# Kernel tuning notes

Measured on AMD Instinct MI355X. Metric: run time of the kernel, lower is better.

The kernel has to match this reference:

```python
import jax, jax.numpy as jnp
import numpy as np

N = 16384   # number of nodes == output_dim
E = 524288  # directed edges (avg degree 32)
IN_DIM, HID = 16, 128


def _glorot(key, shape):
    fan_in = shape[0]
    return jax.random.normal(key, shape, dtype=jnp.float32) / jnp.sqrt(jnp.float32(fan_in))


def setup_inputs() -> dict:
    key = jax.random.key(0)
    ks = jax.random.split(key, 6)
    x = jax.random.normal(ks[0], (N, IN_DIM), dtype=jnp.float32)
    edge_index = jax.random.randint(ks[1], (2, E), 0, N, dtype=jnp.int64)
    return {
        "x": x,
        "edge_index": edge_index,
        "W1": _glorot(ks[2], (IN_DIM, HID)), "b1": jnp.zeros((HID,), jnp.float32),
        "W2": _glorot(ks[3], (HID, HID)),    "b2": jnp.zeros((HID,), jnp.float32),
        "W3": _glorot(ks[4], (HID, HID)),    "b3": jnp.zeros((HID,), jnp.float32),
        "Wfc": _glorot(ks[5], (HID, N)),     "bfc": jnp.zeros((N,), jnp.float32),
    }


def _gcn_conv(x, W, b, src, dst, norm):
    # GCNConv: h = D^{-1/2} (A + I) D^{-1/2} (x @ W) + b
    h = x @ W                              # [N, out]
    msg = h[src] * norm[:, None]           # gather + per-edge scale
    agg = jax.ops.segment_sum(msg, dst, num_segments=N)  # scatter-add to targets
    return agg + b


def reference(x, edge_index, W1, b1, W2, b2, W3, b3, Wfc, bfc):
    # Add self-loops (PyG GCNConv default)
    loop = jnp.arange(N, dtype=edge_index.dtype)
    src = jnp.concatenate([edge_index[0], loop])   # [E+N]
    dst = jnp.concatenate([edge_index[1], loop])
    # Symmetric degree normalization: deg over incoming edges (weight 1)
    deg = jax.ops.segment_sum(jnp.ones_like(dst, dtype=jnp.float32), dst, num_segments=N)
    dinv = jnp.where(deg > 0, jax.lax.rsqrt(deg), 0.0)
    norm = dinv[src] * dinv[dst]                   # [E+N]

    h = jax.nn.relu(_gcn_conv(x, W1, b1, src, dst, norm))
    h = jax.nn.relu(_gcn_conv(h, W2, b2, src, dst, norm))
    h = jax.nn.relu(_gcn_conv(h, W3, b3, src, dst, norm))
    return h @ Wfc + bfc                           # [N, N] logits over nodes
```

## Files before the change

### kernel.cpp

```cpp
#include <hip/hip_runtime.h>

#define N_NODES 16384
#define E_EDGES 524288
#define HID 128

typedef __attribute__((ext_vector_type(8))) short bf16x8;
typedef __attribute__((ext_vector_type(4))) float f32x4;

__device__ __forceinline__ unsigned short f2bf(float x) {
    unsigned u = __builtin_bit_cast(unsigned, x);
    u = u + 0x7fff + ((u >> 16) & 1);
    return (unsigned short)(u >> 16);
}
__device__ __forceinline__ float bf2f(unsigned short h) {
    return __builtin_bit_cast(float, (unsigned)h << 16);
}


__global__ __launch_bounds__(256) void k_zero(int* __restrict__ cnt) {
    int i = blockIdx.x * 256 + threadIdx.x;
    if (i < N_NODES) cnt[i] = 0;
}

__global__ __launch_bounds__(256) void k_count(const int* __restrict__ ei, int* __restrict__ cnt) {
    int e = blockIdx.x * 256 + threadIdx.x;
    if (e < E_EDGES) {
        int d = ei[E_EDGES + e];
        atomicAdd(&cnt[d], 1);
    }
}

__global__ __launch_bounds__(1024) void k_scan(const int* __restrict__ cnt, int* __restrict__ rp,
                                               int* __restrict__ cur, float* __restrict__ dinv) {
    __shared__ int part[1024];
    int t = threadIdx.x;
    int base = t * 16;
    int loc[16];
    int s = 0;
#pragma unroll
    for (int i = 0; i < 16; ++i) { loc[i] = cnt[base + i]; s += loc[i]; }
    part[t] = s;
    __syncthreads();
    for (int off = 1; off < 1024; off <<= 1) {
        int add = (t >= off) ? part[t - off] : 0;
        __syncthreads();
        part[t] += add;
        __syncthreads();
    }
    int excl = (t == 0) ? 0 : part[t - 1];
#pragma unroll
    for (int i = 0; i < 16; ++i) {
        rp[base + i] = excl;
        cur[base + i] = excl;
        dinv[base + i] = rsqrtf((float)(loc[i] + 1));
        excl += loc[i];
    }
    if (t == 1023) rp[N_NODES] = excl;
}

__global__ __launch_bounds__(256) void k_fill(const int* __restrict__ ei, int* __restrict__ cur,
                                              int* __restrict__ eidx) {
    int e = blockIdx.x * 256 + threadIdx.x;
    if (e < E_EDGES) {
        int s = ei[e];
        int d = ei[E_EDGES + e];
        int p = atomicAdd(&cur[d], 1);
        eidx[p] = s;
    }
}


__global__ __launch_bounds__(256) void k_gemm16(const float* __restrict__ X, const float* __restrict__ W,
                                                float* __restrict__ T) {
    __shared__ float sW[16 * 128];
    int t = threadIdx.x;
#pragma unroll
    for (int i = 0; i < 8; ++i) sW[i * 256 + t] = W[i * 256 + t];
    __syncthreads();
    int row = blockIdx.x * 2 + (t >> 7);
    int c = t & 127;
    const float* xr = X + row * 16;
    float acc = 0.f;
#pragma unroll
    for (int k = 0; k < 16; ++k) acc = fmaf(xr[k], sW[k * 128 + c], acc);
    T[row * HID + c] = acc;
}

__global__ __launch_bounds__(256) void k_gemm128(const float* __restrict__ A, const float* __restrict__ W,
                                                 float* __restrict__ T) {
    __shared__ float sA[64][132];
    __shared__ float sW[128][132];
    int t = threadIdx.x;
    int bm = blockIdx.x * 64;
#pragma unroll
    for (int it = 0; it < 8; ++it) {
        int f = it * 256 + t;
        int m = f >> 5, k4 = f & 31;
        *(float4*)(&sA[m][k4 * 4]) = *(const float4*)(A + (bm + m) * HID + k4 * 4);
    }
#pragma unroll
    for (int it = 0; it < 16; ++it) {
        int f = it * 256 + t;
        int k = f >> 5, n4 = f & 31;
        *(float4*)(&sW[k][n4 * 4]) = *(const float4*)(W + k * HID + n4 * 4);
    }
    __syncthreads();
    int tx = t & 15, ty = t >> 4;
    float acc[4][8] = {};
    for (int k4 = 0; k4 < 32; ++k4) {
        float4 a[4], b0[4], b1[4];
#pragma unroll
        for (int i = 0; i < 4; ++i) a[i] = *(const float4*)(&sA[ty * 4 + i][k4 * 4]);
#pragma unroll
        for (int kk = 0; kk < 4; ++kk) {
            b0[kk] = *(const float4*)(&sW[k4 * 4 + kk][tx * 4]);
            b1[kk] = *(const float4*)(&sW[k4 * 4 + kk][tx * 4 + 64]);
        }
#pragma unroll
        for (int kk = 0; kk < 4; ++kk) {
#pragma unroll
            for (int i = 0; i < 4; ++i) {
                float av = reinterpret_cast<const float*>(&a[i])[kk];
#pragma unroll
                for (int j = 0; j < 4; ++j) {
                    acc[i][j]     = fmaf(av, reinterpret_cast<const float*>(&b0[kk])[j], acc[i][j]);
                    acc[i][4 + j] = fmaf(av, reinterpret_cast<const float*>(&b1[kk])[j], acc[i][4 + j]);
                }
            }
        }
    }
#pragma unroll
    for (int i = 0; i < 4; ++i) {
        int row = bm + ty * 4 + i;
        float4 o0, o1;
        o0.x = acc[i][0]; o0.y = acc[i][1]; o0.z = acc[i][2]; o0.w = acc[i][3];
        o1.x = acc[i][4]; o1.y = acc[i][5]; o1.z = acc[i][6]; o1.w = acc[i][7];
        *(float4*)(T + row * HID + tx * 4) = o0;
        *(float4*)(T + row * HID + tx * 4 + 64) = o1;
    }
}

__global__ __launch_bounds__(128) void k_agg(const float* __restrict__ T, const int* __restrict__ rp,
                                             const int* __restrict__ eidx, const float* __restrict__ dinv,
                                             const float* __restrict__ b, float* __restrict__ H) {
    __shared__ int se[128];
    __shared__ float sw[128];
    int i = blockIdx.x;
    int c = threadIdx.x;
    float di = dinv[i];
    float acc = di * T[i * HID + c];
    int beg = rp[i], end = rp[i + 1];
    for (int base = beg; base < end; base += 128) {
        int e = base + c;
        if (e < end) {
            int s = eidx[e];
            se[c] = s;
            sw[c] = dinv[s];
        }
        __syncthreads();
        int n = min(128, end - base);
        for (int j = 0; j < n; ++j) {
            acc += sw[j] * T[se[j] * HID + c];
        }
        __syncthreads();
    }
    float v = fmaf(di, acc, b[c]);
    H[i * HID + c] = fmaxf(v, 0.0f);
}


__global__ __launch_bounds__(256) void k_split_a(const float* __restrict__ A,
                                                 unsigned short* __restrict__ hi,
                                                 unsigned short* __restrict__ lo) {
    int i = (blockIdx.x * 256 + threadIdx.x) * 8;
    float4 v0 = *(const float4*)(A + i);
    float4 v1 = *(const float4*)(A + i + 4);
    float v[8] = {v0.x, v0.y, v0.z, v0.w, v1.x, v1.y, v1.z, v1.w};
    alignas(16) unsigned short hb[8], lb[8];
#pragma unroll
    for (int j = 0; j < 8; ++j) {
        unsigned short h = f2bf(v[j]);
        hb[j] = h;
        lb[j] = f2bf(v[j] - bf2f(h));
    }
    *(uint4*)(hi + i) = *(uint4*)hb;
    *(uint4*)(lo + i) = *(uint4*)lb;
}

__global__ __launch_bounds__(256) void k_split_b(const float* __restrict__ W,
                                                 unsigned short* __restrict__ bhi,
                                                 unsigned short* __restrict__ blo) {
    __shared__ float sm[32][132];
    int t = threadIdx.x;
    int nb = blockIdx.x;
    int kb = blockIdx.y;
#pragma unroll
    for (int i = 0; i < 4; ++i) {
        int idx = i * 256 + t;
        int k = idx >> 5, n4 = idx & 31;
        *(float4*)(&sm[k][n4 * 4]) =
            *(const float4*)(W + (size_t)(kb * 32 + k) * N_NODES + nb * 128 + n4 * 4);
    }
    __syncthreads();
    int n = t >> 1, half = t & 1;
    alignas(16) unsigned short hb[16], lb[16];
#pragma unroll
    for (int j = 0; j < 16; ++j) {
        float x = sm[half * 16 + j][n];
        unsigned short h = f2bf(x);
        hb[j] = h;
        lb[j] = f2bf(x - bf2f(h));
    }
    size_t o = (size_t)(nb * 128 + n) * 128 + kb * 32 + half * 16;
    *(uint4*)(bhi + o) = *(uint4*)hb;
    *(uint4*)(bhi + o + 8) = *(uint4*)(hb + 8);
    *(uint4*)(blo + o) = *(uint4*)lb;
    *(uint4*)(blo + o + 8) = *(uint4*)(lb + 8);
}

__global__ __launch_bounds__(256) void k_fc_mfma(const unsigned short* __restrict__ Ahi,
                                                 const unsigned short* __restrict__ Alo,
                                                 const unsigned short* __restrict__ Bhi,
                                                 const unsigned short* __restrict__ Blo,
                                                 const float* __restrict__ bias,
                                                 float* __restrict__ C) {
    int t = threadIdx.x;
    int wid = t >> 6, lane = t & 63;
    int wm = wid >> 1, wn = wid & 1;
    int row16 = lane & 15, kq = lane >> 4;

    int wg = blockIdx.x;
    int xcd = wg & 7;
    int q = wg >> 3;
    int bn = xcd * 16 + (q & 15);
    int bm = q >> 4;

    int m0 = bm * 128 + wm * 64;
    int n0 = bn * 128 + wn * 64;

    const unsigned short* pah = Ahi + (size_t)(m0 + row16) * HID + kq * 8;
    const unsigned short* pal = Alo + (size_t)(m0 + row16) * HID + kq * 8;
    const unsigned short* pbh = Bhi + (size_t)(n0 + row16) * HID + kq * 8;
    const unsigned short* pbl = Blo + (size_t)(n0 + row16) * HID + kq * 8;

    f32x4 acc[4][4] = {};
#pragma unroll
    for (int ks = 0; ks < 4; ++ks) {
        bf16x8 ah[4], al[4], bh[4], bl[4];
#pragma unroll
        for (int m = 0; m < 4; ++m) {
            ah[m] = *(const bf16x8*)(pah + m * 16 * HID + ks * 32);
            al[m] = *(const bf16x8*)(pal + m * 16 * HID + ks * 32);
        }
#pragma unroll
        for (int n = 0; n < 4; ++n) {
            bh[n] = *(const bf16x8*)(pbh + n * 16 * HID + ks * 32);
            bl[n] = *(const bf16x8*)(pbl + n * 16 * HID + ks * 32);
        }
#pragma unroll
        for (int n = 0; n < 4; ++n) {
#pragma unroll
            for (int m = 0; m < 4; ++m)
                acc[m][n] = __builtin_amdgcn_mfma_f32_16x16x32_bf16(ah[m], bh[n], acc[m][n], 0, 0, 0);
#pragma unroll
            for (int m = 0; m < 4; ++m)
                acc[m][n] = __builtin_amdgcn_mfma_f32_16x16x32_bf16(ah[m], bl[n], acc[m][n], 0, 0, 0);
#pragma unroll
            for (int m = 0; m < 4; ++m)
                acc[m][n] = __builtin_amdgcn_mfma_f32_16x16x32_bf16(al[m], bh[n], acc[m][n], 0, 0, 0);
        }
    }

#pragma unroll
    for (int n = 0; n < 4; ++n) {
        int col = n0 + n * 16 + row16;
        float bv = bias[col];
#pragma unroll
        for (int m = 0; m < 4; ++m) {
            int r0 = m0 + m * 16 + kq * 4;
#pragma unroll
            for (int r = 0; r < 4; ++r)
                __builtin_nontemporal_store(acc[m][n][r] + bv,
                                            C + (size_t)(r0 + r) * N_NODES + col);
        }
    }
}


extern "C" void kernel_launch(void* const* d_in, const int* in_sizes, int n_in,
                              void* d_out, int out_size, void* d_ws, size_t ws_size,
                              hipStream_t stream) {
    const float* x   = (const float*)d_in[0];
    const int*   ei  = (const int*)d_in[1];
    const float* W1  = (const float*)d_in[2];
    const float* b1  = (const float*)d_in[3];
    const float* W2  = (const float*)d_in[4];
    const float* b2  = (const float*)d_in[5];
    const float* W3  = (const float*)d_in[6];
    const float* b3  = (const float*)d_in[7];
    const float* Wfc = (const float*)d_in[8];
    const float* bfc = (const float*)d_in[9];
    float* out = (float*)d_out;

    char* ws = (char*)d_ws;
    int* cnt  = (int*)ws;
    int* rp   = cnt + N_NODES;
    int* cur  = rp + N_NODES + 64;
    int* eidx = cur + N_NODES;
    float* dinv = (float*)(eidx + E_EDGES);
    float* t  = dinv + N_NODES;
    float* h  = t + N_NODES * HID;
    unsigned short* ahi = (unsigned short*)t;
    unsigned short* alo = ahi + N_NODES * HID;
    unsigned short* bhi = (unsigned short*)(h + N_NODES * HID);
    unsigned short* blo = bhi + N_NODES * HID;

    k_zero<<<N_NODES / 256, 256, 0, stream>>>(cnt);
    k_count<<<E_EDGES / 256, 256, 0, stream>>>(ei, cnt);
    k_scan<<<1, 1024, 0, stream>>>(cnt, rp, cur, dinv);
    k_fill<<<E_EDGES / 256, 256, 0, stream>>>(ei, cur, eidx);

    k_gemm16<<<N_NODES / 2, 256, 0, stream>>>(x, W1, t);
    k_agg<<<N_NODES, 128, 0, stream>>>(t, rp, eidx, dinv, b1, h);
    k_gemm128<<<N_NODES / 64, 256, 0, stream>>>(h, W2, t);
    k_agg<<<N_NODES, 128, 0, stream>>>(t, rp, eidx, dinv, b2, h);
    k_gemm128<<<N_NODES / 64, 256, 0, stream>>>(h, W3, t);
    k_agg<<<N_NODES, 128, 0, stream>>>(t, rp, eidx, dinv, b3, h);

    k_split_b<<<dim3(N_NODES / 128, HID / 32), 256, 0, stream>>>(Wfc, bhi, blo);
    k_split_a<<<(N_NODES * HID) / (256 * 8), 256, 0, stream>>>(h, ahi, alo);

    k_fc_mfma<<<N_NODES / 128 * (N_NODES / 128), 256, 0, stream>>>(ahi, alo, bhi, blo, bfc, out);
}
```

Baseline: 709.3 us.

## Make FC GEMM persistent with register-resident A tiles looping over column strips

The final FC GEMM now runs as 512 persistent blocks instead of one block per 128x128 tile. Each wave loads its 64-row A hi/lo slices for the full K into registers once, then loops 32 times over 64-column strips of B, so A is never reloaded. Output stores become ordinary stores instead of nontemporal stores. This adds a lot of register pressure (A fragments plus accumulators), which lowers occupancy and leaves fewer blocks to hide B-load latency.

```diff
diff --git a/kernel.cpp b/kernel.cpp
--- a/kernel.cpp
+++ b/kernel.cpp
@@ -226,62 +226,62 @@
                                                  float* __restrict__ C) {
     int t = threadIdx.x;
     int wid = t >> 6, lane = t & 63;
-    int wm = wid >> 1, wn = wid & 1;
     int row16 = lane & 15, kq = lane >> 4;
 
-    int wg = blockIdx.x;
-    int xcd = wg & 7;
-    int q = wg >> 3;
-    int bn = xcd * 16 + (q & 15);
-    int bm = q >> 4;
-
-    int m0 = bm * 128 + wm * 64;
-    int n0 = bn * 128 + wn * 64;
-
-    const unsigned short* pah = Ahi + (size_t)(m0 + row16) * HID + kq * 8;
-    const unsigned short* pal = Alo + (size_t)(m0 + row16) * HID + kq * 8;
-    const unsigned short* pbh = Bhi + (size_t)(n0 + row16) * HID + kq * 8;
-    const unsigned short* pbl = Blo + (size_t)(n0 + row16) * HID + kq * 8;
-
-    f32x4 acc[4][4] = {};
-#pragma unroll
-    for (int ks = 0; ks < 4; ++ks) {
-        bf16x8 ah[4], al[4], bh[4], bl[4];
-#pragma unroll
-        for (int m = 0; m < 4; ++m) {
-            ah[m] = *(const bf16x8*)(pah + m * 16 * HID + ks * 32);
-            al[m] = *(const bf16x8*)(pal + m * 16 * HID + ks * 32);
-        }
+    int m0 = (blockIdx.x >> 3) * 256;
+    int colbase = (blockIdx.x & 7) * 2048;
+    int mrow0 = m0 + wid * 64;
+
+    const unsigned short* pah = Ahi + (size_t)(mrow0 + row16) * HID + kq * 8;
+    const unsigned short* pal = Alo + (size_t)(mrow0 + row16) * HID + kq * 8;
+    bf16x8 ahp[4][4], alp[4][4];
+#pragma unroll
+    for (int m = 0; m < 4; ++m)
+#pragma unroll
+        for (int ks = 0; ks < 4; ++ks) {
+            ahp[m][ks] = *(const bf16x8*)(pah + m * 16 * HID + ks * 32);
+            alp[m][ks] = *(const bf16x8*)(pal + m * 16 * HID + ks * 32);
+        }
+
+    for (int it = 0; it < 32; ++it) {
+        int n0 = colbase + it * 64;
+        const unsigned short* pbh = Bhi + (size_t)(n0 + row16) * HID + kq * 8;
+        const unsigned short* pbl = Blo + (size_t)(n0 + row16) * HID + kq * 8;
+
+        f32x4 acc[4][4] = {};
+#pragma unroll
+        for (int ks = 0; ks < 4; ++ks) {
+            bf16x8 bh[4], bl[4];
+#pragma unroll
+            for (int n = 0; n < 4; ++n) {
+                bh[n] = *(const bf16x8*)(pbh + n * 16 * HID + ks * 32);
+                bl[n] = *(const bf16x8*)(pbl + n * 16 * HID + ks * 32);
+            }
+#pragma unroll
+            for (int n = 0; n < 4; ++n) {
+#pragma unroll
+                for (int m = 0; m < 4; ++m)
+                    acc[m][n] = __builtin_amdgcn_mfma_f32_16x16x32_bf16(ahp[m][ks], bh[n], acc[m][n], 0, 0, 0);
+#pragma unroll
+                for (int m = 0; m < 4; ++m)
+                    acc[m][n] = __builtin_amdgcn_mfma_f32_16x16x32_bf16(ahp[m][ks], bl[n], acc[m][n], 0, 0, 0);
+#pragma unroll
+                for (int m = 0; m < 4; ++m)
+                    acc[m][n] = __builtin_amdgcn_mfma_f32_16x16x32_bf16(alp[m][ks], bh[n], acc[m][n], 0, 0, 0);
+            }
+        }
+
 #pragma unroll
         for (int n = 0; n < 4; ++n) {
-            bh[n] = *(const bf16x8*)(pbh + n * 16 * HID + ks * 32);
-            bl[n] = *(const bf16x8*)(pbl + n * 16 * HID + ks * 32);
-        }
-#pragma unroll
-        for (int n = 0; n < 4; ++n) {
-#pragma unroll
-            for (int m = 0; m < 4; ++m)
-                acc[m][n] = __builtin_amdgcn_mfma_f32_16x16x32_bf16(ah[m], bh[n], acc[m][n], 0, 0, 0);
-#pragma unroll
-            for (int m = 0; m < 4; ++m)
-                acc[m][n] = __builtin_amdgcn_mfma_f32_16x16x32_bf16(ah[m], bl[n], acc[m][n], 0, 0, 0);
-#pragma unroll
-            for (int m = 0; m < 4; ++m)
-                acc[m][n] = __builtin_amdgcn_mfma_f32_16x16x32_bf16(al[m], bh[n], acc[m][n], 0, 0, 0);
-        }
-    }
-
-#pragma unroll
-    for (int n = 0; n < 4; ++n) {
-        int col = n0 + n * 16 + row16;
-        float bv = bias[col];
-#pragma unroll
-        for (int m = 0; m < 4; ++m) {
-            int r0 = m0 + m * 16 + kq * 4;
-#pragma unroll
-            for (int r = 0; r < 4; ++r)
-                __builtin_nontemporal_store(acc[m][n][r] + bv,
-                                            C + (size_t)(r0 + r) * N_NODES + col);
+            int col = n0 + n * 16 + row16;
+            float bv = bias[col];
+#pragma unroll
+            for (int m = 0; m < 4; ++m) {
+                int r0 = mrow0 + m * 16 + kq * 4;
+#pragma unroll
+                for (int r = 0; r < 4; ++r)
+                    C[(size_t)(r0 + r) * N_NODES + col] = acc[m][n][r] + bv;
+            }
         }
     }
 }
@@ -330,5 +330,5 @@
     k_split_b<<<dim3(N_NODES / 128, HID / 32), 256, 0, stream>>>(Wfc, bhi, blo);
     k_split_a<<<(N_NODES * HID) / (256 * 8), 256, 0, stream>>>(h, ahi, alo);
 
-    k_fc_mfma<<<N_NODES / 128 * (N_NODES / 128), 256, 0, stream>>>(ahi, alo, bhi, blo, bfc, out);
-}
+    k_fc_mfma<<<512, 256, 0, stream>>>(ahi, alo, bhi, blo, bfc, out);
+}
```

Result: slower. 1.031 ms (+45.4%).

## Stage FC GEMM operands through LDS with concatenated split-bf16 K dimension

Applied to the files above, without the earlier changes.

The split-bf16 hi/lo operands are repacked into single arrays with a tripled K dimension (hi,hi,lo times hi,lo,hi), so the three-product emulation becomes one plain GEMM with K=384. The FC kernel now loads 128x64 tiles into padded shared memory with register prefetch of the next stage, instead of each wave reading fragments straight from global memory. Nontemporal output stores become plain stores, and the XCD-aware block swizzle is replaced by a simple row-major mapping. This adds extra workspace writes during prep and LDS synchronisation, and may change L2 locality.

```diff
diff --git a/kernel.cpp b/kernel.cpp
--- a/kernel.cpp
+++ b/kernel.cpp
@@ -3,6 +3,8 @@
 #define N_NODES 16384
 #define E_EDGES 524288
 #define HID 128
+#define KP 384
+#define PADK 72
 
 typedef __attribute__((ext_vector_type(8))) short bf16x8;
 typedef __attribute__((ext_vector_type(4))) float f32x4;
@@ -168,13 +170,12 @@
     H[i * HID + c] = fmaxf(v, 0.0f);
 }
 
-
-__global__ __launch_bounds__(256) void k_split_a(const float* __restrict__ A,
-                                                 unsigned short* __restrict__ hi,
-                                                 unsigned short* __restrict__ lo) {
-    int i = (blockIdx.x * 256 + threadIdx.x) * 8;
-    float4 v0 = *(const float4*)(A + i);
-    float4 v1 = *(const float4*)(A + i + 4);
+__global__ __launch_bounds__(256) void k_prep_a2(const float* __restrict__ A,
+                                                 unsigned short* __restrict__ A2) {
+    int idx = (blockIdx.x * 256 + threadIdx.x) * 8;
+    int r = idx >> 7, k = idx & 127;
+    float4 v0 = *(const float4*)(A + idx);
+    float4 v1 = *(const float4*)(A + idx + 4);
     float v[8] = {v0.x, v0.y, v0.z, v0.w, v1.x, v1.y, v1.z, v1.w};
     alignas(16) unsigned short hb[8], lb[8];
 #pragma unroll
@@ -183,13 +184,14 @@
         hb[j] = h;
         lb[j] = f2bf(v[j] - bf2f(h));
     }
-    *(uint4*)(hi + i) = *(uint4*)hb;
-    *(uint4*)(lo + i) = *(uint4*)lb;
-}
-
-__global__ __launch_bounds__(256) void k_split_b(const float* __restrict__ W,
-                                                 unsigned short* __restrict__ bhi,
-                                                 unsigned short* __restrict__ blo) {
+    size_t o = (size_t)r * KP + k;
+    *(uint4*)(A2 + o)       = *(uint4*)hb;
+    *(uint4*)(A2 + o + 128) = *(uint4*)hb;
+    *(uint4*)(A2 + o + 256) = *(uint4*)lb;
+}
+
+__global__ __launch_bounds__(256) void k_prep_b2(const float* __restrict__ W,
+                                                 unsigned short* __restrict__ B2) {
     __shared__ float sm[32][132];
     int t = threadIdx.x;
     int nb = blockIdx.x;
@@ -211,66 +213,74 @@
         hb[j] = h;
         lb[j] = f2bf(x - bf2f(h));
     }
-    size_t o = (size_t)(nb * 128 + n) * 128 + kb * 32 + half * 16;
-    *(uint4*)(bhi + o) = *(uint4*)hb;
-    *(uint4*)(bhi + o + 8) = *(uint4*)(hb + 8);
-    *(uint4*)(blo + o) = *(uint4*)lb;
-    *(uint4*)(blo + o + 8) = *(uint4*)(lb + 8);
-}
-
-__global__ __launch_bounds__(256) void k_fc_mfma(const unsigned short* __restrict__ Ahi,
-                                                 const unsigned short* __restrict__ Alo,
-                                                 const unsigned short* __restrict__ Bhi,
-                                                 const unsigned short* __restrict__ Blo,
-                                                 const float* __restrict__ bias,
-                                                 float* __restrict__ C) {
-    int t = threadIdx.x;
+    size_t o = (size_t)(nb * 128 + n) * KP + kb * 32 + half * 16;
+    *(uint4*)(B2 + o)           = *(uint4*)hb;
+    *(uint4*)(B2 + o + 8)       = *(uint4*)(hb + 8);
+    *(uint4*)(B2 + o + 128)     = *(uint4*)lb;
+    *(uint4*)(B2 + o + 136)     = *(uint4*)(lb + 8);
+    *(uint4*)(B2 + o + 256)     = *(uint4*)hb;
+    *(uint4*)(B2 + o + 264)     = *(uint4*)(hb + 8);
+}
+
+__global__ __launch_bounds__(256, 3) void k_fc_mfma(const unsigned short* __restrict__ A2,
+                                                    const unsigned short* __restrict__ B2,
+                                                    const float* __restrict__ bias,
+                                                    float* __restrict__ C) {
+    __shared__ unsigned short sA[128 * PADK];
+    __shared__ unsigned short sB[128 * PADK];
+    int t = threadIdx.x;
+    int bn = blockIdx.x & 127, bm = blockIdx.x >> 7;
     int wid = t >> 6, lane = t & 63;
     int wm = wid >> 1, wn = wid & 1;
     int row16 = lane & 15, kq = lane >> 4;
 
-    int wg = blockIdx.x;
-    int xcd = wg & 7;
-    int q = wg >> 3;
-    int bn = xcd * 16 + (q & 15);
-    int bm = q >> 4;
+    int sR = t >> 3, sk8 = t & 7;
+    const unsigned short* gA = A2 + (size_t)(bm * 128 + sR) * KP + sk8 * 8;
+    const unsigned short* gB = B2 + (size_t)(bn * 128 + sR) * KP + sk8 * 8;
+
+    uint4 ga[4], gb[4];
+#pragma unroll
+    for (int i = 0; i < 4; ++i) {
+        ga[i] = *(const uint4*)(gA + (size_t)i * 32 * KP);
+        gb[i] = *(const uint4*)(gB + (size_t)i * 32 * KP);
+    }
+
+    f32x4 acc[4][4] = {};
+#pragma unroll
+    for (int s = 0; s < 6; ++s) {
+#pragma unroll
+        for (int i = 0; i < 4; ++i) {
+            *(uint4*)(&sA[(sR + i * 32) * PADK + sk8 * 8]) = ga[i];
+            *(uint4*)(&sB[(sR + i * 32) * PADK + sk8 * 8]) = gb[i];
+        }
+        __syncthreads();
+        if (s < 5) {
+#pragma unroll
+            for (int i = 0; i < 4; ++i) {
+                ga[i] = *(const uint4*)(gA + (s + 1) * 64 + (size_t)i * 32 * KP);
+                gb[i] = *(const uint4*)(gB + (s + 1) * 64 + (size_t)i * 32 * KP);
+            }
+        }
+#pragma unroll
+        for (int kk = 0; kk < 2; ++kk) {
+            bf16x8 af[4], bf[4];
+#pragma unroll
+            for (int m = 0; m < 4; ++m)
+                af[m] = *(const bf16x8*)(&sA[(wm * 64 + m * 16 + row16) * PADK + kk * 32 + kq * 8]);
+#pragma unroll
+            for (int n = 0; n < 4; ++n)
+                bf[n] = *(const bf16x8*)(&sB[(wn * 64 + n * 16 + row16) * PADK + kk * 32 + kq * 8]);
+#pragma unroll
+            for (int n = 0; n < 4; ++n)
+#pragma unroll
+                for (int m = 0; m < 4; ++m)
+                    acc[m][n] = __builtin_amdgcn_mfma_f32_16x16x32_bf16(af[m], bf[n], acc[m][n], 0, 0, 0);
+        }
+        __syncthreads();
+    }
 
     int m0 = bm * 128 + wm * 64;
     int n0 = bn * 128 + wn * 64;
-
-    const unsigned short* pah = Ahi + (size_t)(m0 + row16) * HID + kq * 8;
-    const unsigned short* pal = Alo + (size_t)(m0 + row16) * HID + kq * 8;
-    const unsigned short* pbh = Bhi + (size_t)(n0 + row16) * HID + kq * 8;
-    const unsigned short* pbl = Blo + (size_t)(n0 + row16) * HID + kq * 8;
-
-    f32x4 acc[4][4] = {};
-#pragma unroll
-    for (int ks = 0; ks < 4; ++ks) {
-        bf16x8 ah[4], al[4], bh[4], bl[4];
-#pragma unroll
-        for (int m = 0; m < 4; ++m) {
-            ah[m] = *(const bf16x8*)(pah + m * 16 * HID + ks * 32);
-            al[m] = *(const bf16x8*)(pal + m * 16 * HID + ks * 32);
-        }
-#pragma unroll
-        for (int n = 0; n < 4; ++n) {
-            bh[n] = *(const bf16x8*)(pbh + n * 16 * HID + ks * 32);
-            bl[n] = *(const bf16x8*)(pbl + n * 16 * HID + ks * 32);
-        }
-#pragma unroll
-        for (int n = 0; n < 4; ++n) {
-#pragma unroll
-            for (int m = 0; m < 4; ++m)
-                acc[m][n] = __builtin_amdgcn_mfma_f32_16x16x32_bf16(ah[m], bh[n], acc[m][n], 0, 0, 0);
-#pragma unroll
-            for (int m = 0; m < 4; ++m)
-                acc[m][n] = __builtin_amdgcn_mfma_f32_16x16x32_bf16(ah[m], bl[n], acc[m][n], 0, 0, 0);
-#pragma unroll
-            for (int m = 0; m < 4; ++m)
-                acc[m][n] = __builtin_amdgcn_mfma_f32_16x16x32_bf16(al[m], bh[n], acc[m][n], 0, 0, 0);
-        }
-    }
-
 #pragma unroll
     for (int n = 0; n < 4; ++n) {
         int col = n0 + n * 16 + row16;
@@ -280,8 +290,7 @@
             int r0 = m0 + m * 16 + kq * 4;
 #pragma unroll
             for (int r = 0; r < 4; ++r)
-                __builtin_nontemporal_store(acc[m][n][r] + bv,
-                                            C + (size_t)(r0 + r) * N_NODES + col);
+                C[(size_t)(r0 + r) * N_NODES + col] = acc[m][n][r] + bv;
         }
     }
 }
@@ -310,10 +319,8 @@
     float* dinv = (float*)(eidx + E_EDGES);
     float* t  = dinv + N_NODES;
     float* h  = t + N_NODES * HID;
-    unsigned short* ahi = (unsigned short*)t;
-    unsigned short* alo = ahi + N_NODES * HID;
-    unsigned short* bhi = (unsigned short*)(h + N_NODES * HID);
-    unsigned short* blo = bhi + N_NODES * HID;
+    unsigned short* A2 = (unsigned short*)(h + N_NODES * HID);
+    unsigned short* B2 = A2 + (size_t)N_NODES * KP;
 
     k_zero<<<N_NODES / 256, 256, 0, stream>>>(cnt);
     k_count<<<E_EDGES / 256, 256, 0, stream>>>(ei, cnt);
@@ -327,8 +334,8 @@
     k_gemm128<<<N_NODES / 64, 256, 0, stream>>>(h, W3, t);
     k_agg<<<N_NODES, 128, 0, stream>>>(t, rp, eidx, dinv, b3, h);
 
-    k_split_b<<<dim3(N_NODES / 128, HID / 32), 256, 0, stream>>>(Wfc, bhi, blo);
-    k_split_a<<<(N_NODES * HID) / (256 * 8), 256, 0, stream>>>(h, ahi, alo);
-
-    k_fc_mfma<<<N_NODES / 128 * (N_NODES / 128), 256, 0, stream>>>(ahi, alo, bhi, blo, bfc, out);
-}
+    k_prep_b2<<<dim3(N_NODES / 128, HID / 32), 256, 0, stream>>>(Wfc, B2);
+    k_prep_a2<<<(N_NODES * HID) / (256 * 8), 256, 0, stream>>>(h, A2);
+
+    k_fc_mfma<<<N_NODES / 128 * (N_NODES / 128), 256, 0, stream>>>(A2, B2, bfc, out);
+}
```

New measurement: 1.570 ms. +121.4%, slower.
